# Performance work log

Measured on AMD Instinct MI355X. Metric: run time of the kernel, lower is better.

## Reference

```python
import jax, jax.numpy as jnp
import numpy as np

B, L, H, C = 1, 512, 1024, 2


def setup_inputs() -> dict:
    key = jax.random.key(0)
    k1, k2, k3 = jax.random.split(key, 3)
    lm_output = jax.random.normal(k1, (B, L, H), dtype=jnp.float32)
    # torch Linear weight layout: [out_features, in_features]
    W1 = jax.random.normal(k2, (H, 2 * H), dtype=jnp.float32) * 0.02
    b1 = jnp.zeros((H,), dtype=jnp.float32)
    W2 = jax.random.normal(k3, (C, H), dtype=jnp.float32) * 0.02
    b2 = jnp.zeros((C,), dtype=jnp.float32)
    return {"lm_output": lm_output, "W1": W1, "b1": b1, "W2": W2, "b2": b2}


def reference(lm_output, W1, b1, W2, b2):
    # pair_emb[b,i,j] = concat(lm_output[b,j], lm_output[b,i])
    # Linear(concat(a,b)) decomposes: split W1 into the halves acting on each part.
    Wa = W1[:, :H]  # acts on lm_output_a (the j / column token)
    Wb = W1[:, H:]  # acts on lm_output_b (the i / row token)
    a_proj = jnp.einsum('blh,oh->blo', lm_output, Wa)  # [B,L,H]
    b_proj = jnp.einsum('blh,oh->blo', lm_output, Wb)  # [B,L,H]
    # hidden[b,i,j] = tanh(a_proj[b,j] + b_proj[b,i] + b1)   -> [B,L,L,H]
    hidden = jnp.tanh(a_proj[:, None, :, :] + b_proj[:, :, None, :] + b1)
    # Dropout is identity at inference time.
    logits = jnp.einsum('bijh,ch->bijc', hidden, W2) + b2  # [B,L,L,C]
    logits = (logits + jnp.swapaxes(logits, 1, 2)) / 2.0
    return logits
```

## Files before the change

kernel.cpp:

```cpp
#include <hip/hip_runtime.h>
#include <hip/hip_bf16.h>

#define HH 1024
#define LL 512
#define NT 16
#define NTRI 136

typedef __attribute__((ext_vector_type(8))) short bf16x8;
typedef __attribute__((ext_vector_type(4))) float f32x4;
typedef __attribute__((ext_vector_type(2))) float f32x2;

static constexpr float C_EXP = 2.8853900817779268f;

static __device__ __forceinline__ uint4 pack8(float4 a, float4 b) {
    union { uint4 u; __hip_bfloat162 h[4]; } r;
    r.h[0] = __float22bfloat162_rn(make_float2(a.x, a.y));
    r.h[1] = __float22bfloat162_rn(make_float2(a.z, a.w));
    r.h[2] = __float22bfloat162_rn(make_float2(b.x, b.y));
    r.h[3] = __float22bfloat162_rn(make_float2(b.z, b.w));
    return r.u;
}

__global__ __launch_bounds__(256, 4) void proj_mfma_kernel(
    const float* __restrict__ lm, const float* __restrict__ W1,
    const float* __restrict__ b1, float* __restrict__ Ea, float* __restrict__ Eb)
{
    __shared__ ushort As[64][136];
    __shared__ ushort Bs[64][136];

    const int tid  = threadIdx.x;
    const int lane = tid & 63;
    const int w    = tid >> 6;
    const int b    = blockIdx.x;
    const int xcd  = b & 7;
    const int idx  = b >> 3;
    const int nbase = (xcd * 4 + (idx & 3)) * 64;
    const int mbase = (idx >> 2) * 64;
    const int wm   = w * 16;
    const int sel  = nbase >> 10;
    const int nrow = nbase & 1023;

    const int frow = lane & 15;
    const int q8   = (lane >> 4) * 8;

    f32x4 acc[4] = {};

    for (int kb = 0; kb < HH; kb += 128) {
        __syncthreads();
        {
            int p = tid;
#pragma unroll
            for (int it = 0; it < 4; ++it, p += 256) {
                const int row = p >> 4, c8 = (p & 15) * 8;
                const float* pa = &lm[(mbase + row) * HH + kb + c8];
                *(uint4*)&As[row][c8] = pack8(*(const float4*)pa, *(const float4*)(pa + 4));
                const float* pw = &W1[(nrow + row) * 2048 + sel * 1024 + kb + c8];
                *(uint4*)&Bs[row][c8] = pack8(*(const float4*)pw, *(const float4*)(pw + 4));
            }
        }
        __syncthreads();

#pragma unroll
        for (int s = 0; s < 4; ++s) {
            const bf16x8 a = *(const bf16x8*)&As[wm + frow][s * 32 + q8];
#pragma unroll
            for (int nf = 0; nf < 4; ++nf) {
                const bf16x8 bb = *(const bf16x8*)&Bs[nf * 16 + frow][s * 32 + q8];
                acc[nf] = __builtin_amdgcn_mfma_f32_16x16x32_bf16(a, bb, acc[nf], 0, 0, 0);
            }
        }
    }

    const int col = lane & 15;
    const int rq  = (lane >> 4) * 4;
    const int m0  = mbase + wm + rq;
    const bool isA = sel == 0;
#pragma unroll
    for (int nf = 0; nf < 4; ++nf) {
        const int nn = (nrow + nf * 16 + col);
        if (isA) {
            const float bb = b1[nn];
#pragma unroll
            for (int r = 0; r < 4; ++r)
                Ea[(m0 + r) * HH + nn] = __builtin_amdgcn_exp2f(C_EXP * (acc[nf][r] + bb));
        } else {
#pragma unroll
            for (int r = 0; r < 4; ++r)
                Eb[(m0 + r) * HH + nn] = __builtin_amdgcn_exp2f(C_EXP * acc[nf][r]);
        }
    }
}

__global__ __launch_bounds__(256, 5) void pair_kernel(
    const float* __restrict__ Ea, const float* __restrict__ Eb,
    const float* __restrict__ W2, float* __restrict__ pbuf, int slice)
{
    __shared__ float tl[4][32][64];

    const int tid = threadIdx.x;
    const int tx  = tid & 15;
    const int ty  = tid >> 4;

    int tt = blockIdx.x, bi = 0, rem = NT;
    while (tt >= rem) { tt -= rem; --rem; ++bi; }
    const int bj    = bi + tt;
    const int ibase = bi * 32;
    const int jbase = bj * 32;
    const int k0    = blockIdx.y * slice;

    f32x2 aC0[2] = {}, aC1[2] = {};
    const f32x2 one2 = {1.f, 1.f};

    for (int kb = 0; kb < slice; kb += 64) {
        if (kb) __syncthreads();
        {
            int p = tid;
#pragma unroll
            for (int it = 0; it < 8; ++it, p += 256) {
                const int tile = p >> 9;
                const int row  = (p >> 4) & 31;
                const int c4   = p & 15;
                float4 v;
                if      (tile == 0) v = *(const float4*)&Ea[(jbase + row) * HH + k0 + kb + c4 * 4];
                else if (tile == 1) v = *(const float4*)&Ea[(ibase + row) * HH + k0 + kb + c4 * 4];
                else if (tile == 2) v = *(const float4*)&Eb[(ibase + row) * HH + k0 + kb + c4 * 4];
                else                v = *(const float4*)&Eb[(jbase + row) * HH + k0 + kb + c4 * 4];
                const int c4s = (tile == 0 || tile == 3) ? (c4 ^ (row & 15)) : c4;
                *(float4*)&tl[tile][row][c4s * 4] = v;
            }
        }
        __syncthreads();

#pragma unroll 4
        for (int h4 = 0; h4 < 16; ++h4) {
            const int sx = (h4 ^ tx) * 4;
            const float4 Aj0 = *(const float4*)&tl[0][tx][sx];
            const float4 Aj1 = *(const float4*)&tl[0][tx + 16][sx];
            const float4 Bj0 = *(const float4*)&tl[3][tx][sx];
            const float4 Bj1 = *(const float4*)&tl[3][tx + 16][sx];
            const float4 Ai0 = *(const float4*)&tl[1][ty][h4 * 4];
            const float4 Ai1 = *(const float4*)&tl[1][ty + 16][h4 * 4];
            const float4 Bi0 = *(const float4*)&tl[2][ty][h4 * 4];
            const float4 Bi1 = *(const float4*)&tl[2][ty + 16][h4 * 4];
            const float4 w0q = *(const float4*)&W2[k0 + kb + h4 * 4];
            const float4 w1q = *(const float4*)&W2[HH + k0 + kb + h4 * 4];

#define DO_H(AJ0v, AJ1v, BI0v, BI1v, AI0v, AI1v, BJ0v, BJ1v, W0s, W1s)        \
            {                                                                  \
                const f32x2 Aj = {AJ0v, AJ1v};                                 \
                const f32x2 Bj = {BJ0v, BJ1v};                                 \
                const f32x2 d0 = __builtin_elementwise_fma((f32x2){BI0v, BI0v}, Aj, one2); \
                const f32x2 d1 = __builtin_elementwise_fma((f32x2){BI1v, BI1v}, Aj, one2); \
                const f32x2 e0 = __builtin_elementwise_fma((f32x2){AI0v, AI0v}, Bj, one2); \
                const f32x2 e1 = __builtin_elementwise_fma((f32x2){AI1v, AI1v}, Bj, one2); \
                const float dp0 = d0.x * d0.y, dp1 = d1.x * d1.y;              \
                const float ep0 = e0.x * e0.y, ep1 = e1.x * e1.y;              \
                const float DR = __builtin_amdgcn_rcpf(dp0 * dp1);             \
                const float ER = __builtin_amdgcn_rcpf(ep0 * ep1);             \
                const f32x2 dq = (f32x2){DR, DR} * (f32x2){dp1, dp0};          \
                const f32x2 eq = (f32x2){ER, ER} * (f32x2){ep1, ep0};          \
                const f32x2 u0 = (f32x2){dq.x, dq.x} * d0.yx + (f32x2){eq.x, eq.x} * e0.yx; \
                const f32x2 u1 = (f32x2){dq.y, dq.y} * d1.yx + (f32x2){eq.y, eq.y} * e1.yx; \
                aC0[0] = __builtin_elementwise_fma(u0, (f32x2){(W0s), (W0s)}, aC0[0]); \
                aC1[0] = __builtin_elementwise_fma(u0, (f32x2){(W1s), (W1s)}, aC1[0]); \
                aC0[1] = __builtin_elementwise_fma(u1, (f32x2){(W0s), (W0s)}, aC0[1]); \
                aC1[1] = __builtin_elementwise_fma(u1, (f32x2){(W1s), (W1s)}, aC1[1]); \
            }
            DO_H(Aj0.x, Aj1.x, Bi0.x, Bi1.x, Ai0.x, Ai1.x, Bj0.x, Bj1.x, w0q.x, w1q.x)
            DO_H(Aj0.y, Aj1.y, Bi0.y, Bi1.y, Ai0.y, Ai1.y, Bj0.y, Bj1.y, w0q.y, w1q.y)
            DO_H(Aj0.z, Aj1.z, Bi0.z, Bi1.z, Ai0.z, Ai1.z, Bj0.z, Bj1.z, w0q.z, w1q.z)
            DO_H(Aj0.w, Aj1.w, Bi0.w, Bi1.w, Ai0.w, Ai1.w, Bj0.w, Bj1.w, w0q.w, w1q.w)
#undef DO_H
        }
    }

    float* pb = pbuf + ((size_t)blockIdx.y * NTRI + blockIdx.x) * 2048;
#pragma unroll
    for (int ii = 0; ii < 2; ++ii)
#pragma unroll
        for (int jj = 0; jj < 2; ++jj) {
            const int li = ty + ii * 16, lj = tx + jj * 16;
            const f32x2 v = { jj ? aC0[ii].y : aC0[ii].x,
                              jj ? aC1[ii].y : aC1[ii].x };
            *(f32x2*)&pb[(li * 32 + lj) * 2] = v;
        }
}

__global__ __launch_bounds__(256) void combine_kernel(
    const float* __restrict__ pbuf, const float* __restrict__ W2,
    const float* __restrict__ b2, float* __restrict__ out, int nz)
{
    __shared__ float s_ws[2];

    const int tid = threadIdx.x;
    if (tid < 128) {
        const int c = tid >> 6, l = tid & 63;
        float s = 0.f;
#pragma unroll
        for (int q = 0; q < 4; ++q) {
            const float4 v = *(const float4*)&W2[c * HH + (l + q * 64) * 4];
            s += v.x + v.y + v.z + v.w;
        }
#pragma unroll
        for (int off = 32; off; off >>= 1) s += __shfl_down(s, off, 64);
        if (l == 0) s_ws[c] = s + b2[c];
    }
    __syncthreads();

    const int idx   = blockIdx.x * 256 + tid;
    const int t     = idx >> 11;
    const int local = idx & 2047;
    int tt = t, bi = 0, rem = NT;
    while (tt >= rem) { tt -= rem; --rem; ++bi; }
    const int bj = bi + tt;

    float s0 = 0.f, s1 = 0.f;
    for (int z = 0; z < nz; z += 2) {
        s0 += pbuf[((size_t)z * NTRI + t) * 2048 + local];
        s1 += pbuf[((size_t)(z + 1) * NTRI + t) * 2048 + local];
    }
    const float s = s0 + s1;

    const int li = local >> 6;
    const int lj = (local >> 1) & 31;
    const int c  = local & 1;
    const float v = s_ws[c] - s;

    const int i = bi * 32 + li;
    const int j = bj * 32 + lj;
    out[(i * LL + j) * 2 + c] = v;
    out[(j * LL + i) * 2 + c] = v;
}

extern "C" void kernel_launch(void* const* d_in, const int* in_sizes, int n_in,
                              void* d_out, int out_size, void* d_ws, size_t ws_size,
                              hipStream_t stream)
{
    const float* lm = (const float*)d_in[0];
    const float* W1 = (const float*)d_in[1];
    const float* b1 = (const float*)d_in[2];
    const float* W2 = (const float*)d_in[3];
    const float* b2 = (const float*)d_in[4];
    float* out = (float*)d_out;

    char* ws = (char*)d_ws;
    float* Ea   = (float*)ws;
    float* Eb   = (float*)(ws + (2u << 20));
    float* pbuf = (float*)(ws + (4u << 20) + 64);

    const size_t ubase = (4u << 20) + 64;
    const size_t pb16  = (size_t)16 * NTRI * 2048 * 4;
    const int nz = (ws_size >= ubase + pb16) ? 16 : 8;
    const int slice = HH / nz;

    proj_mfma_kernel<<<256, 256, 0, stream>>>(lm, W1, b1, Ea, Eb);
    pair_kernel<<<dim3(NTRI, nz), 256, 0, stream>>>(Ea, Eb, W2, pbuf, slice);
    combine_kernel<<<(NTRI * 2048) / 256, 256, 0, stream>>>(pbuf, W2, b2, out, nz);
}
```

Before: 129.2 us.

## Enlarge pair tiles to 64x64 with 4x4 register blocking and merged reciprocal

The pair kernel now uses 64x64 triangular tiles (36 tiles) with each thread holding a 4x4 block of pair outputs, where before it used 32x32 tiles (136) with 2x2 per thread. This raises arithmetic reuse per shared-memory load. The tanh-sum formula is regrouped so one reciprocal covers four h values for the symmetric pair. The K split can now go up to 32 slices depending on workspace size, and the combine kernel sums four partials at a time. The cost is higher register pressure (occupancy hint lowered to 3), fewer blocks per slice, and a larger partial buffer for the combine pass to read.

```diff
diff --git a/kernel.cpp b/kernel.cpp
--- a/kernel.cpp
+++ b/kernel.cpp
@@ -3,8 +3,8 @@
 
 #define HH 1024
 #define LL 512
-#define NT 16
-#define NTRI 136
+#define TNT 8
+#define NTILE 36
 
 typedef __attribute__((ext_vector_type(8))) short bf16x8;
 typedef __attribute__((ext_vector_type(4))) float f32x4;
@@ -20,6 +20,9 @@
     r.h[3] = __float22bfloat162_rn(make_float2(b.z, b.w));
     return r.u;
 }
+
+static __device__ __forceinline__ f32x2 lo2(const float4& v) { return (f32x2){v.x, v.y}; }
+static __device__ __forceinline__ f32x2 hi2(const float4& v) { return (f32x2){v.z, v.w}; }
 
 __global__ __launch_bounds__(256, 4) void proj_mfma_kernel(
     const float* __restrict__ lm, const float* __restrict__ W1,
@@ -91,98 +94,105 @@
     }
 }
 
-__global__ __launch_bounds__(256, 5) void pair_kernel(
+__global__ __launch_bounds__(256, 3) void pair_kernel(
     const float* __restrict__ Ea, const float* __restrict__ Eb,
     const float* __restrict__ W2, float* __restrict__ pbuf, int slice)
 {
-    __shared__ float tl[4][32][64];
+    __shared__ float tl[4][64][32];
 
     const int tid = threadIdx.x;
     const int tx  = tid & 15;
     const int ty  = tid >> 4;
 
-    int tt = blockIdx.x, bi = 0, rem = NT;
+    int tt = blockIdx.x, bi = 0, rem = TNT;
     while (tt >= rem) { tt -= rem; --rem; ++bi; }
     const int bj    = bi + tt;
-    const int ibase = bi * 32;
-    const int jbase = bj * 32;
+    const int ibase = bi * 64;
+    const int jbase = bj * 64;
     const int k0    = blockIdx.y * slice;
 
-    f32x2 aC0[2] = {}, aC1[2] = {};
+    f32x2 acc0[4][4] = {};
+    f32x2 acc1[4][4] = {};
     const f32x2 one2 = {1.f, 1.f};
 
-    for (int kb = 0; kb < slice; kb += 64) {
+    for (int kb = 0; kb < slice; kb += 32) {
         if (kb) __syncthreads();
         {
-            int p = tid;
-#pragma unroll
-            for (int it = 0; it < 8; ++it, p += 256) {
-                const int tile = p >> 9;
-                const int row  = (p >> 4) & 31;
-                const int c4   = p & 15;
-                float4 v;
-                if      (tile == 0) v = *(const float4*)&Ea[(jbase + row) * HH + k0 + kb + c4 * 4];
-                else if (tile == 1) v = *(const float4*)&Ea[(ibase + row) * HH + k0 + kb + c4 * 4];
-                else if (tile == 2) v = *(const float4*)&Eb[(ibase + row) * HH + k0 + kb + c4 * 4];
-                else                v = *(const float4*)&Eb[(jbase + row) * HH + k0 + kb + c4 * 4];
-                const int c4s = (tile == 0 || tile == 3) ? (c4 ^ (row & 15)) : c4;
-                *(float4*)&tl[tile][row][c4s * 4] = v;
+            const int c4  = tid & 7;
+            const int r0  = tid >> 3;
+            const int hof = k0 + kb + c4 * 4;
+#pragma unroll
+            for (int it = 0; it < 8; ++it) {
+                const int tile = it >> 1;
+                const int row  = (it & 1) * 32 + r0;
+                const int base = (tile < 2) ? jbase : ibase;
+                const float* src = (tile == 0 || tile == 2) ? Ea : Eb;
+                const int c4s = c4 ^ (row & 7);
+                *(float4*)&tl[tile][row][c4s * 4] =
+                    *(const float4*)&src[(size_t)(base + row) * HH + hof];
             }
         }
         __syncthreads();
 
-#pragma unroll 4
-        for (int h4 = 0; h4 < 16; ++h4) {
-            const int sx = (h4 ^ tx) * 4;
-            const float4 Aj0 = *(const float4*)&tl[0][tx][sx];
-            const float4 Aj1 = *(const float4*)&tl[0][tx + 16][sx];
-            const float4 Bj0 = *(const float4*)&tl[3][tx][sx];
-            const float4 Bj1 = *(const float4*)&tl[3][tx + 16][sx];
-            const float4 Ai0 = *(const float4*)&tl[1][ty][h4 * 4];
-            const float4 Ai1 = *(const float4*)&tl[1][ty + 16][h4 * 4];
-            const float4 Bi0 = *(const float4*)&tl[2][ty][h4 * 4];
-            const float4 Bi1 = *(const float4*)&tl[2][ty + 16][h4 * 4];
+#pragma unroll 2
+        for (int h4 = 0; h4 < 8; ++h4) {
+            const int sxj = (h4 ^ (tx & 7)) * 4;
+            const int sxi = (h4 ^ (ty & 7)) * 4;
+            float4 Aj[4], Bj[4], Ai[4], Bi[4];
+#pragma unroll
+            for (int jj = 0; jj < 4; ++jj) {
+                Aj[jj] = *(const float4*)&tl[0][tx + 16 * jj][sxj];
+                Bj[jj] = *(const float4*)&tl[1][tx + 16 * jj][sxj];
+            }
+#pragma unroll
+            for (int ii = 0; ii < 4; ++ii) {
+                Ai[ii] = *(const float4*)&tl[2][ty + 16 * ii][sxi];
+                Bi[ii] = *(const float4*)&tl[3][ty + 16 * ii][sxi];
+            }
             const float4 w0q = *(const float4*)&W2[k0 + kb + h4 * 4];
             const float4 w1q = *(const float4*)&W2[HH + k0 + kb + h4 * 4];
-
-#define DO_H(AJ0v, AJ1v, BI0v, BI1v, AI0v, AI1v, BJ0v, BJ1v, W0s, W1s)        \
-            {                                                                  \
-                const f32x2 Aj = {AJ0v, AJ1v};                                 \
-                const f32x2 Bj = {BJ0v, BJ1v};                                 \
-                const f32x2 d0 = __builtin_elementwise_fma((f32x2){BI0v, BI0v}, Aj, one2); \
-                const f32x2 d1 = __builtin_elementwise_fma((f32x2){BI1v, BI1v}, Aj, one2); \
-                const f32x2 e0 = __builtin_elementwise_fma((f32x2){AI0v, AI0v}, Bj, one2); \
-                const f32x2 e1 = __builtin_elementwise_fma((f32x2){AI1v, AI1v}, Bj, one2); \
-                const float dp0 = d0.x * d0.y, dp1 = d1.x * d1.y;              \
-                const float ep0 = e0.x * e0.y, ep1 = e1.x * e1.y;              \
-                const float DR = __builtin_amdgcn_rcpf(dp0 * dp1);             \
-                const float ER = __builtin_amdgcn_rcpf(ep0 * ep1);             \
-                const f32x2 dq = (f32x2){DR, DR} * (f32x2){dp1, dp0};          \
-                const f32x2 eq = (f32x2){ER, ER} * (f32x2){ep1, ep0};          \
-                const f32x2 u0 = (f32x2){dq.x, dq.x} * d0.yx + (f32x2){eq.x, eq.x} * e0.yx; \
-                const f32x2 u1 = (f32x2){dq.y, dq.y} * d1.yx + (f32x2){eq.y, eq.y} * e1.yx; \
-                aC0[0] = __builtin_elementwise_fma(u0, (f32x2){(W0s), (W0s)}, aC0[0]); \
-                aC1[0] = __builtin_elementwise_fma(u0, (f32x2){(W1s), (W1s)}, aC1[0]); \
-                aC0[1] = __builtin_elementwise_fma(u1, (f32x2){(W0s), (W0s)}, aC0[1]); \
-                aC1[1] = __builtin_elementwise_fma(u1, (f32x2){(W1s), (W1s)}, aC1[1]); \
-            }
-            DO_H(Aj0.x, Aj1.x, Bi0.x, Bi1.x, Ai0.x, Ai1.x, Bj0.x, Bj1.x, w0q.x, w1q.x)
-            DO_H(Aj0.y, Aj1.y, Bi0.y, Bi1.y, Ai0.y, Ai1.y, Bj0.y, Bj1.y, w0q.y, w1q.y)
-            DO_H(Aj0.z, Aj1.z, Bi0.z, Bi1.z, Ai0.z, Ai1.z, Bj0.z, Bj1.z, w0q.z, w1q.z)
-            DO_H(Aj0.w, Aj1.w, Bi0.w, Bi1.w, Ai0.w, Ai1.w, Bj0.w, Bj1.w, w0q.w, w1q.w)
-#undef DO_H
-        }
-    }
-
-    float* pb = pbuf + ((size_t)blockIdx.y * NTRI + blockIdx.x) * 2048;
-#pragma unroll
-    for (int ii = 0; ii < 2; ++ii)
-#pragma unroll
-        for (int jj = 0; jj < 2; ++jj) {
-            const int li = ty + ii * 16, lj = tx + jj * 16;
-            const f32x2 v = { jj ? aC0[ii].y : aC0[ii].x,
-                              jj ? aC1[ii].y : aC1[ii].x };
-            *(f32x2*)&pb[(li * 32 + lj) * 2] = v;
+            const f32x2 w0lo = lo2(w0q), w0hi = hi2(w0q);
+            const f32x2 w1lo = lo2(w1q), w1hi = hi2(w1q);
+
+#pragma unroll
+            for (int ii = 0; ii < 4; ++ii) {
+                const f32x2 ailo = lo2(Ai[ii]), aihi = hi2(Ai[ii]);
+                const f32x2 bilo = lo2(Bi[ii]), bihi = hi2(Bi[ii]);
+#pragma unroll
+                for (int jj = 0; jj < 4; ++jj) {
+                    const f32x2 d01 = __builtin_elementwise_fma(bilo, lo2(Aj[jj]), one2);
+                    const f32x2 d23 = __builtin_elementwise_fma(bihi, hi2(Aj[jj]), one2);
+                    const f32x2 e01 = __builtin_elementwise_fma(ailo, lo2(Bj[jj]), one2);
+                    const f32x2 e23 = __builtin_elementwise_fma(aihi, hi2(Bj[jj]), one2);
+                    const f32x2 n01 = d01 + e01, n23 = d23 + e23;
+                    const f32x2 m01 = d01 * e01, m23 = d23 * e23;
+                    const float p01 = m01.x * m01.y;
+                    const float p23 = m23.x * m23.y;
+                    const float R   = __builtin_amdgcn_rcpf(p01 * p23);
+                    const float r01 = R * p23;
+                    const float r23 = R * p01;
+                    const f32x2 u01 = (n01 * __builtin_shufflevector(m01, m01, 1, 0))
+                                      * (f32x2){r01, r01};
+                    const f32x2 u23 = (n23 * __builtin_shufflevector(m23, m23, 1, 0))
+                                      * (f32x2){r23, r23};
+                    acc0[ii][jj] = __builtin_elementwise_fma(u01, w0lo, acc0[ii][jj]);
+                    acc0[ii][jj] = __builtin_elementwise_fma(u23, w0hi, acc0[ii][jj]);
+                    acc1[ii][jj] = __builtin_elementwise_fma(u01, w1lo, acc1[ii][jj]);
+                    acc1[ii][jj] = __builtin_elementwise_fma(u23, w1hi, acc1[ii][jj]);
+                }
+            }
+        }
+    }
+
+    float* pb = pbuf + ((size_t)blockIdx.y * NTILE + blockIdx.x) * 8192;
+#pragma unroll
+    for (int ii = 0; ii < 4; ++ii)
+#pragma unroll
+        for (int jj = 0; jj < 4; ++jj) {
+            const int li = ty + 16 * ii, lj = tx + 16 * jj;
+            const f32x2 v = { acc0[ii][jj].x + acc0[ii][jj].y,
+                              acc1[ii][jj].x + acc1[ii][jj].y };
+            *(f32x2*)&pb[(li * 64 + lj) * 2] = v;
         }
 }
 
@@ -208,26 +218,28 @@
     __syncthreads();
 
     const int idx   = blockIdx.x * 256 + tid;
-    const int t     = idx >> 11;
-    const int local = idx & 2047;
-    int tt = t, bi = 0, rem = NT;
+    const int t     = idx >> 13;
+    const int local = idx & 8191;
+    int tt = t, bi = 0, rem = TNT;
     while (tt >= rem) { tt -= rem; --rem; ++bi; }
     const int bj = bi + tt;
 
-    float s0 = 0.f, s1 = 0.f;
-    for (int z = 0; z < nz; z += 2) {
-        s0 += pbuf[((size_t)z * NTRI + t) * 2048 + local];
-        s1 += pbuf[((size_t)(z + 1) * NTRI + t) * 2048 + local];
-    }
-    const float s = s0 + s1;
-
-    const int li = local >> 6;
-    const int lj = (local >> 1) & 31;
+    float s0 = 0.f, s1 = 0.f, s2 = 0.f, s3 = 0.f;
+    for (int z = 0; z < nz; z += 4) {
+        s0 += pbuf[((size_t)z * NTILE + t) * 8192 + local];
+        s1 += pbuf[((size_t)(z + 1) * NTILE + t) * 8192 + local];
+        s2 += pbuf[((size_t)(z + 2) * NTILE + t) * 8192 + local];
+        s3 += pbuf[((size_t)(z + 3) * NTILE + t) * 8192 + local];
+    }
+    const float s = (s0 + s1) + (s2 + s3);
+
+    const int li = local >> 7;
+    const int lj = (local >> 1) & 63;
     const int c  = local & 1;
     const float v = s_ws[c] - s;
 
-    const int i = bi * 32 + li;
-    const int j = bj * 32 + lj;
+    const int i = bi * 64 + li;
+    const int j = bj * 64 + lj;
     out[(i * LL + j) * 2 + c] = v;
     out[(j * LL + i) * 2 + c] = v;
 }
@@ -249,11 +261,13 @@
     float* pbuf = (float*)(ws + (4u << 20) + 64);
 
     const size_t ubase = (4u << 20) + 64;
-    const size_t pb16  = (size_t)16 * NTRI * 2048 * 4;
-    const int nz = (ws_size >= ubase + pb16) ? 16 : 8;
+    const size_t per_z = (size_t)NTILE * 8192 * 4;
+    int nz = 8;
+    if      (ws_size >= ubase + 32 * per_z) nz = 32;
+    else if (ws_size >= ubase + 16 * per_z) nz = 16;
     const int slice = HH / nz;
 
     proj_mfma_kernel<<<256, 256, 0, stream>>>(lm, W1, b1, Ea, Eb);
-    pair_kernel<<<dim3(NTRI, nz), 256, 0, stream>>>(Ea, Eb, W2, pbuf, slice);
-    combine_kernel<<<(NTRI * 2048) / 256, 256, 0, stream>>>(pbuf, W2, b2, out, nz);
-}
+    pair_kernel<<<dim3(NTILE, nz), 256, 0, stream>>>(Ea, Eb, W2, pbuf, slice);
+    combine_kernel<<<(NTILE * 8192) / 256, 256, 0, stream>>>(pbuf, W2, b2, out, nz);
+}
```

Measured after the change: 129.2 us. Within noise of the previous version (-0.0%).

## Regroup tanh-sum algebra per pair and halve projection tile width

Applied to the files above, without the earlier changes.

The pair kernel now computes, for each (i,j) pair, the sum of the two symmetric tanh terms as (d+e)/(d*e), with d and e the two exponential products. One reciprocal is shared across four h values and the paired-vector f32x2 formulation is replaced by scalar accumulators. This is meant to cut the multiplies and reciprocals per hidden element in the dominant loop. Separately, the projection kernel uses 32-wide N tiles and launches 512 blocks instead of 256 to raise parallelism, at the cost of reloading the A tile more often. Pair-kernel occupancy hint and unroll factor are also lowered.

```diff
diff --git a/kernel.cpp b/kernel.cpp
--- a/kernel.cpp
+++ b/kernel.cpp
@@ -26,7 +26,7 @@
     const float* __restrict__ b1, float* __restrict__ Ea, float* __restrict__ Eb)
 {
     __shared__ ushort As[64][136];
-    __shared__ ushort Bs[64][136];
+    __shared__ ushort Bs[32][136];
 
     const int tid  = threadIdx.x;
     const int lane = tid & 63;
@@ -34,8 +34,8 @@
     const int b    = blockIdx.x;
     const int xcd  = b & 7;
     const int idx  = b >> 3;
-    const int nbase = (xcd * 4 + (idx & 3)) * 64;
-    const int mbase = (idx >> 2) * 64;
+    const int nbase = (xcd * 8 + (idx & 7)) * 32;
+    const int mbase = (idx >> 3) * 64;
     const int wm   = w * 16;
     const int sel  = nbase >> 10;
     const int nrow = nbase & 1023;
@@ -43,7 +43,7 @@
     const int frow = lane & 15;
     const int q8   = (lane >> 4) * 8;
 
-    f32x4 acc[4] = {};
+    f32x4 acc[2] = {};
 
     for (int kb = 0; kb < HH; kb += 128) {
         __syncthreads();
@@ -54,6 +54,11 @@
                 const int row = p >> 4, c8 = (p & 15) * 8;
                 const float* pa = &lm[(mbase + row) * HH + kb + c8];
                 *(uint4*)&As[row][c8] = pack8(*(const float4*)pa, *(const float4*)(pa + 4));
+            }
+            int q = tid;
+#pragma unroll
+            for (int it = 0; it < 2; ++it, q += 256) {
+                const int row = q >> 4, c8 = (q & 15) * 8;
                 const float* pw = &W1[(nrow + row) * 2048 + sel * 1024 + kb + c8];
                 *(uint4*)&Bs[row][c8] = pack8(*(const float4*)pw, *(const float4*)(pw + 4));
             }
@@ -64,7 +69,7 @@
         for (int s = 0; s < 4; ++s) {
             const bf16x8 a = *(const bf16x8*)&As[wm + frow][s * 32 + q8];
 #pragma unroll
-            for (int nf = 0; nf < 4; ++nf) {
+            for (int nf = 0; nf < 2; ++nf) {
                 const bf16x8 bb = *(const bf16x8*)&Bs[nf * 16 + frow][s * 32 + q8];
                 acc[nf] = __builtin_amdgcn_mfma_f32_16x16x32_bf16(a, bb, acc[nf], 0, 0, 0);
             }
@@ -76,7 +81,7 @@
     const int m0  = mbase + wm + rq;
     const bool isA = sel == 0;
 #pragma unroll
-    for (int nf = 0; nf < 4; ++nf) {
+    for (int nf = 0; nf < 2; ++nf) {
         const int nn = (nrow + nf * 16 + col);
         if (isA) {
             const float bb = b1[nn];
@@ -91,7 +96,7 @@
     }
 }
 
-__global__ __launch_bounds__(256, 5) void pair_kernel(
+__global__ __launch_bounds__(256, 4) void pair_kernel(
     const float* __restrict__ Ea, const float* __restrict__ Eb,
     const float* __restrict__ W2, float* __restrict__ pbuf, int slice)
 {
@@ -108,8 +113,8 @@
     const int jbase = bj * 32;
     const int k0    = blockIdx.y * slice;
 
-    f32x2 aC0[2] = {}, aC1[2] = {};
-    const f32x2 one2 = {1.f, 1.f};
+    float a00_0 = 0.f, a00_1 = 0.f, a01_0 = 0.f, a01_1 = 0.f;
+    float a10_0 = 0.f, a10_1 = 0.f, a11_0 = 0.f, a11_1 = 0.f;
 
     for (int kb = 0; kb < slice; kb += 64) {
         if (kb) __syncthreads();
@@ -131,7 +136,7 @@
         }
         __syncthreads();
 
-#pragma unroll 4
+#pragma unroll 2
         for (int h4 = 0; h4 < 16; ++h4) {
             const int sx = (h4 ^ tx) * 4;
             const float4 Aj0 = *(const float4*)&tl[0][tx][sx];
@@ -145,45 +150,46 @@
             const float4 w0q = *(const float4*)&W2[k0 + kb + h4 * 4];
             const float4 w1q = *(const float4*)&W2[HH + k0 + kb + h4 * 4];
 
-#define DO_H(AJ0v, AJ1v, BI0v, BI1v, AI0v, AI1v, BJ0v, BJ1v, W0s, W1s)        \
-            {                                                                  \
-                const f32x2 Aj = {AJ0v, AJ1v};                                 \
-                const f32x2 Bj = {BJ0v, BJ1v};                                 \
-                const f32x2 d0 = __builtin_elementwise_fma((f32x2){BI0v, BI0v}, Aj, one2); \
-                const f32x2 d1 = __builtin_elementwise_fma((f32x2){BI1v, BI1v}, Aj, one2); \
-                const f32x2 e0 = __builtin_elementwise_fma((f32x2){AI0v, AI0v}, Bj, one2); \
-                const f32x2 e1 = __builtin_elementwise_fma((f32x2){AI1v, AI1v}, Bj, one2); \
-                const float dp0 = d0.x * d0.y, dp1 = d1.x * d1.y;              \
-                const float ep0 = e0.x * e0.y, ep1 = e1.x * e1.y;              \
-                const float DR = __builtin_amdgcn_rcpf(dp0 * dp1);             \
-                const float ER = __builtin_amdgcn_rcpf(ep0 * ep1);             \
-                const f32x2 dq = (f32x2){DR, DR} * (f32x2){dp1, dp0};          \
-                const f32x2 eq = (f32x2){ER, ER} * (f32x2){ep1, ep0};          \
-                const f32x2 u0 = (f32x2){dq.x, dq.x} * d0.yx + (f32x2){eq.x, eq.x} * e0.yx; \
-                const f32x2 u1 = (f32x2){dq.y, dq.y} * d1.yx + (f32x2){eq.y, eq.y} * e1.yx; \
-                aC0[0] = __builtin_elementwise_fma(u0, (f32x2){(W0s), (W0s)}, aC0[0]); \
-                aC1[0] = __builtin_elementwise_fma(u0, (f32x2){(W1s), (W1s)}, aC1[0]); \
-                aC0[1] = __builtin_elementwise_fma(u1, (f32x2){(W0s), (W0s)}, aC0[1]); \
-                aC1[1] = __builtin_elementwise_fma(u1, (f32x2){(W1s), (W1s)}, aC1[1]); \
-            }
-            DO_H(Aj0.x, Aj1.x, Bi0.x, Bi1.x, Ai0.x, Ai1.x, Bj0.x, Bj1.x, w0q.x, w1q.x)
-            DO_H(Aj0.y, Aj1.y, Bi0.y, Bi1.y, Ai0.y, Ai1.y, Bj0.y, Bj1.y, w0q.y, w1q.y)
-            DO_H(Aj0.z, Aj1.z, Bi0.z, Bi1.z, Ai0.z, Ai1.z, Bj0.z, Bj1.z, w0q.z, w1q.z)
-            DO_H(Aj0.w, Aj1.w, Bi0.w, Bi1.w, Ai0.w, Ai1.w, Bj0.w, Bj1.w, w0q.w, w1q.w)
-#undef DO_H
+#define PAIR(AIv, BIv, AJv, BJv, A0, A1)                                        \
+            {                                                                    \
+                const float d0 = fmaf(BIv.x, AJv.x, 1.f);                        \
+                const float d1 = fmaf(BIv.y, AJv.y, 1.f);                        \
+                const float d2 = fmaf(BIv.z, AJv.z, 1.f);                        \
+                const float d3 = fmaf(BIv.w, AJv.w, 1.f);                        \
+                const float e0 = fmaf(AIv.x, BJv.x, 1.f);                        \
+                const float e1 = fmaf(AIv.y, BJv.y, 1.f);                        \
+                const float e2 = fmaf(AIv.z, BJv.z, 1.f);                        \
+                const float e3 = fmaf(AIv.w, BJv.w, 1.f);                        \
+                const float m0 = d0 * e0, m1 = d1 * e1;                          \
+                const float m2 = d2 * e2, m3 = d3 * e3;                          \
+                const float n0 = d0 + e0, n1 = d1 + e1;                          \
+                const float n2 = d2 + e2, n3 = d3 + e3;                          \
+                const float t01 = m0 * m1, t23 = m2 * m3;                        \
+                const float R  = __builtin_amdgcn_rcpf(t01 * t23);               \
+                const float Ra = R * t23, Rb = R * t01;                          \
+                const float q0 = n0 * m1 * Ra, q1 = n1 * m0 * Ra;                \
+                const float q2 = n2 * m3 * Rb, q3 = n3 * m2 * Rb;                \
+                A0 = fmaf(q0, w0q.x, fmaf(q1, w0q.y,                             \
+                     fmaf(q2, w0q.z, fmaf(q3, w0q.w, A0))));                     \
+                A1 = fmaf(q0, w1q.x, fmaf(q1, w1q.y,                             \
+                     fmaf(q2, w1q.z, fmaf(q3, w1q.w, A1))));                     \
+            }
+            PAIR(Ai0, Bi0, Aj0, Bj0, a00_0, a00_1)
+            PAIR(Ai0, Bi0, Aj1, Bj1, a01_0, a01_1)
+            PAIR(Ai1, Bi1, Aj0, Bj0, a10_0, a10_1)
+            PAIR(Ai1, Bi1, Aj1, Bj1, a11_0, a11_1)
+#undef PAIR
         }
     }
 
     float* pb = pbuf + ((size_t)blockIdx.y * NTRI + blockIdx.x) * 2048;
-#pragma unroll
-    for (int ii = 0; ii < 2; ++ii)
-#pragma unroll
-        for (int jj = 0; jj < 2; ++jj) {
-            const int li = ty + ii * 16, lj = tx + jj * 16;
-            const f32x2 v = { jj ? aC0[ii].y : aC0[ii].x,
-                              jj ? aC1[ii].y : aC1[ii].x };
-            *(f32x2*)&pb[(li * 32 + lj) * 2] = v;
-        }
+    {
+        const int li0 = ty, li1 = ty + 16, lj0 = tx, lj1 = tx + 16;
+        *(f32x2*)&pb[(li0 * 32 + lj0) * 2] = (f32x2){a00_0, a00_1};
+        *(f32x2*)&pb[(li0 * 32 + lj1) * 2] = (f32x2){a01_0, a01_1};
+        *(f32x2*)&pb[(li1 * 32 + lj0) * 2] = (f32x2){a10_0, a10_1};
+        *(f32x2*)&pb[(li1 * 32 + lj1) * 2] = (f32x2){a11_0, a11_1};
+    }
 }
 
 __global__ __launch_bounds__(256) void combine_kernel(
@@ -253,7 +259,7 @@
     const int nz = (ws_size >= ubase + pb16) ? 16 : 8;
     const int slice = HH / nz;
 
-    proj_mfma_kernel<<<256, 256, 0, stream>>>(lm, W1, b1, Ea, Eb);
+    proj_mfma_kernel<<<512, 256, 0, stream>>>(lm, W1, b1, Ea, Eb);
     pair_kernel<<<dim3(NTRI, nz), 256, 0, stream>>>(Ea, Eb, W2, pbuf, slice);
     combine_kernel<<<(NTRI * 2048) / 256, 256, 0, stream>>>(pbuf, W2, b2, out, nz);
 }
```

Result: no change. 129.9 us (+0.6%).

## Shrink projection and pair tiles, add register prefetch in projection GEMM

Applied to the files above, without the earlier changes.

The projection GEMM moves from 64x64 tiles with K-step 128 to 32x32 tiles with K-step 64. It launches four times as many blocks and prefetches the next K-slab into registers while the current slab is computed. The pair kernel halves its shared-memory K-chunk to 32, applies a matching XOR swizzle to all four tiles, and raises its occupancy hint. Together these aim to improve occupancy and latency hiding. In exchange they add more barriers and less reuse per block, and nz is now hard-coded to 16 with no check on workspace size.

```diff
diff --git a/kernel.cpp b/kernel.cpp
--- a/kernel.cpp
+++ b/kernel.cpp
@@ -5,6 +5,7 @@
 #define LL 512
 #define NT 16
 #define NTRI 136
+#define NZ 16
 
 typedef __attribute__((ext_vector_type(8))) short bf16x8;
 typedef __attribute__((ext_vector_type(4))) float f32x4;
@@ -12,7 +13,7 @@
 
 static constexpr float C_EXP = 2.8853900817779268f;
 
-static __device__ __forceinline__ uint4 pack8(float4 a, float4 b) {
+static __device__ __forceinline__ uint4 pack8(f32x4 a, f32x4 b) {
     union { uint4 u; __hip_bfloat162 h[4]; } r;
     r.h[0] = __float22bfloat162_rn(make_float2(a.x, a.y));
     r.h[1] = __float22bfloat162_rn(make_float2(a.z, a.w));
@@ -21,12 +22,12 @@
     return r.u;
 }
 
-__global__ __launch_bounds__(256, 4) void proj_mfma_kernel(
+__global__ __launch_bounds__(256, 8) void proj_mfma_kernel(
     const float* __restrict__ lm, const float* __restrict__ W1,
     const float* __restrict__ b1, float* __restrict__ Ea, float* __restrict__ Eb)
 {
-    __shared__ ushort As[64][136];
-    __shared__ ushort Bs[64][136];
+    __shared__ ushort As[32][72];
+    __shared__ ushort Bs[32][72];
 
     const int tid  = threadIdx.x;
     const int lane = tid & 63;
@@ -34,68 +35,74 @@
     const int b    = blockIdx.x;
     const int xcd  = b & 7;
     const int idx  = b >> 3;
-    const int nbase = (xcd * 4 + (idx & 3)) * 64;
-    const int mbase = (idx >> 2) * 64;
-    const int wm   = w * 16;
+    const int nbase = (xcd * 8 + (idx & 7)) * 32;
+    const int mbase = (idx >> 3) * 32;
+    const int wm   = (w & 1) * 16;
+    const int wn   = (w >> 1) * 16;
     const int sel  = nbase >> 10;
     const int nrow = nbase & 1023;
 
     const int frow = lane & 15;
     const int q8   = (lane >> 4) * 8;
 
-    f32x4 acc[4] = {};
-
-    for (int kb = 0; kb < HH; kb += 128) {
+    const int r0a = tid >> 3;
+    const int c8  = (tid & 7) * 8;
+
+    f32x4 acc = {};
+    f32x4 ld[2][2];
+
+#define PLOAD(kb)                                                              \
+    {                                                                          \
+        const float* pa = &lm[(mbase + r0a) * HH + (kb) + c8];                 \
+        const float* pw = &W1[(nrow + r0a) * 2048 + sel * 1024 + (kb) + c8];   \
+        ld[0][0] = *(const f32x4*)pa; ld[0][1] = *(const f32x4*)(pa + 4);      \
+        ld[1][0] = *(const f32x4*)pw; ld[1][1] = *(const f32x4*)(pw + 4);      \
+    }
+
+#define PSTORE()                                                               \
+    {                                                                          \
+        *(uint4*)&As[r0a][c8] = pack8(ld[0][0], ld[0][1]);                     \
+        *(uint4*)&Bs[r0a][c8] = pack8(ld[1][0], ld[1][1]);                     \
+    }
+
+    PLOAD(0)
+    for (int kb = 0; kb < HH; kb += 64) {
         __syncthreads();
-        {
-            int p = tid;
-#pragma unroll
-            for (int it = 0; it < 4; ++it, p += 256) {
-                const int row = p >> 4, c8 = (p & 15) * 8;
-                const float* pa = &lm[(mbase + row) * HH + kb + c8];
-                *(uint4*)&As[row][c8] = pack8(*(const float4*)pa, *(const float4*)(pa + 4));
-                const float* pw = &W1[(nrow + row) * 2048 + sel * 1024 + kb + c8];
-                *(uint4*)&Bs[row][c8] = pack8(*(const float4*)pw, *(const float4*)(pw + 4));
-            }
-        }
+        PSTORE()
+        if (kb + 64 < HH) PLOAD(kb + 64)
         __syncthreads();
 
 #pragma unroll
-        for (int s = 0; s < 4; ++s) {
-            const bf16x8 a = *(const bf16x8*)&As[wm + frow][s * 32 + q8];
-#pragma unroll
-            for (int nf = 0; nf < 4; ++nf) {
-                const bf16x8 bb = *(const bf16x8*)&Bs[nf * 16 + frow][s * 32 + q8];
-                acc[nf] = __builtin_amdgcn_mfma_f32_16x16x32_bf16(a, bb, acc[nf], 0, 0, 0);
-            }
-        }
-    }
+        for (int s = 0; s < 2; ++s) {
+            const bf16x8 a  = *(const bf16x8*)&As[wm + frow][s * 32 + q8];
+            const bf16x8 bb = *(const bf16x8*)&Bs[wn + frow][s * 32 + q8];
+            acc = __builtin_amdgcn_mfma_f32_16x16x32_bf16(a, bb, acc, 0, 0, 0);
+        }
+    }
+#undef PSTORE
+#undef PLOAD
 
     const int col = lane & 15;
     const int rq  = (lane >> 4) * 4;
     const int m0  = mbase + wm + rq;
-    const bool isA = sel == 0;
-#pragma unroll
-    for (int nf = 0; nf < 4; ++nf) {
-        const int nn = (nrow + nf * 16 + col);
-        if (isA) {
-            const float bb = b1[nn];
-#pragma unroll
-            for (int r = 0; r < 4; ++r)
-                Ea[(m0 + r) * HH + nn] = __builtin_amdgcn_exp2f(C_EXP * (acc[nf][r] + bb));
-        } else {
-#pragma unroll
-            for (int r = 0; r < 4; ++r)
-                Eb[(m0 + r) * HH + nn] = __builtin_amdgcn_exp2f(C_EXP * acc[nf][r]);
-        }
-    }
-}
-
-__global__ __launch_bounds__(256, 5) void pair_kernel(
+    const int nn  = nrow + wn + col;
+    if (sel == 0) {
+        const float bb = b1[nn];
+#pragma unroll
+        for (int r = 0; r < 4; ++r)
+            Ea[(m0 + r) * HH + nn] = __builtin_amdgcn_exp2f(C_EXP * (acc[r] + bb));
+    } else {
+#pragma unroll
+        for (int r = 0; r < 4; ++r)
+            Eb[(m0 + r) * HH + nn] = __builtin_amdgcn_exp2f(C_EXP * acc[r]);
+    }
+}
+
+__global__ __launch_bounds__(256, 6) void pair_kernel(
     const float* __restrict__ Ea, const float* __restrict__ Eb,
     const float* __restrict__ W2, float* __restrict__ pbuf, int slice)
 {
-    __shared__ float tl[4][32][64];
+    __shared__ float tl[4][32][32];
 
     const int tid = threadIdx.x;
     const int tx  = tid & 15;
@@ -111,39 +118,34 @@
     f32x2 aC0[2] = {}, aC1[2] = {};
     const f32x2 one2 = {1.f, 1.f};
 
-    for (int kb = 0; kb < slice; kb += 64) {
+    for (int kb = 0; kb < slice; kb += 32) {
         if (kb) __syncthreads();
         {
-            int p = tid;
-#pragma unroll
-            for (int it = 0; it < 8; ++it, p += 256) {
-                const int tile = p >> 9;
-                const int row  = (p >> 4) & 31;
-                const int c4   = p & 15;
-                float4 v;
-                if      (tile == 0) v = *(const float4*)&Ea[(jbase + row) * HH + k0 + kb + c4 * 4];
-                else if (tile == 1) v = *(const float4*)&Ea[(ibase + row) * HH + k0 + kb + c4 * 4];
-                else if (tile == 2) v = *(const float4*)&Eb[(ibase + row) * HH + k0 + kb + c4 * 4];
-                else                v = *(const float4*)&Eb[(jbase + row) * HH + k0 + kb + c4 * 4];
-                const int c4s = (tile == 0 || tile == 3) ? (c4 ^ (row & 15)) : c4;
-                *(float4*)&tl[tile][row][c4s * 4] = v;
-            }
+            const int row = tid >> 3;
+            const int c4  = tid & 7;
+            const int c4s = c4 ^ (row & 7);
+            const int hof = k0 + kb + c4 * 4;
+            *(f32x4*)&tl[0][row][c4s * 4] = *(const f32x4*)&Ea[(jbase + row) * HH + hof];
+            *(f32x4*)&tl[1][row][c4s * 4] = *(const f32x4*)&Ea[(ibase + row) * HH + hof];
+            *(f32x4*)&tl[2][row][c4s * 4] = *(const f32x4*)&Eb[(ibase + row) * HH + hof];
+            *(f32x4*)&tl[3][row][c4s * 4] = *(const f32x4*)&Eb[(jbase + row) * HH + hof];
         }
         __syncthreads();
 
 #pragma unroll 4
-        for (int h4 = 0; h4 < 16; ++h4) {
-            const int sx = (h4 ^ tx) * 4;
-            const float4 Aj0 = *(const float4*)&tl[0][tx][sx];
-            const float4 Aj1 = *(const float4*)&tl[0][tx + 16][sx];
-            const float4 Bj0 = *(const float4*)&tl[3][tx][sx];
-            const float4 Bj1 = *(const float4*)&tl[3][tx + 16][sx];
-            const float4 Ai0 = *(const float4*)&tl[1][ty][h4 * 4];
-            const float4 Ai1 = *(const float4*)&tl[1][ty + 16][h4 * 4];
-            const float4 Bi0 = *(const float4*)&tl[2][ty][h4 * 4];
-            const float4 Bi1 = *(const float4*)&tl[2][ty + 16][h4 * 4];
-            const float4 w0q = *(const float4*)&W2[k0 + kb + h4 * 4];
-            const float4 w1q = *(const float4*)&W2[HH + k0 + kb + h4 * 4];
+        for (int h4 = 0; h4 < 8; ++h4) {
+            const int sx  = (h4 ^ (tx & 7)) * 4;
+            const int sxi = (h4 ^ (ty & 7)) * 4;
+            const f32x4 Aj0 = *(const f32x4*)&tl[0][tx][sx];
+            const f32x4 Aj1 = *(const f32x4*)&tl[0][tx + 16][sx];
+            const f32x4 Bj0 = *(const f32x4*)&tl[3][tx][sx];
+            const f32x4 Bj1 = *(const f32x4*)&tl[3][tx + 16][sx];
+            const f32x4 Ai0 = *(const f32x4*)&tl[1][ty][sxi];
+            const f32x4 Ai1 = *(const f32x4*)&tl[1][ty + 16][sxi];
+            const f32x4 Bi0 = *(const f32x4*)&tl[2][ty][sxi];
+            const f32x4 Bi1 = *(const f32x4*)&tl[2][ty + 16][sxi];
+            const f32x4 w0q = *(const f32x4*)&W2[k0 + kb + h4 * 4];
+            const f32x4 w1q = *(const f32x4*)&W2[HH + k0 + kb + h4 * 4];
 
 #define DO_H(AJ0v, AJ1v, BI0v, BI1v, AI0v, AI1v, BJ0v, BJ1v, W0s, W1s)        \
             {                                                                  \
@@ -159,8 +161,10 @@
                 const float ER = __builtin_amdgcn_rcpf(ep0 * ep1);             \
                 const f32x2 dq = (f32x2){DR, DR} * (f32x2){dp1, dp0};          \
                 const f32x2 eq = (f32x2){ER, ER} * (f32x2){ep1, ep0};          \
-                const f32x2 u0 = (f32x2){dq.x, dq.x} * d0.yx + (f32x2){eq.x, eq.x} * e0.yx; \
-                const f32x2 u1 = (f32x2){dq.y, dq.y} * d1.yx + (f32x2){eq.y, eq.y} * e1.yx; \
+                const f32x2 u0 = (f32x2){dq.x, dq.x} * __builtin_shufflevector(d0, d0, 1, 0) \
+                               + (f32x2){eq.x, eq.x} * __builtin_shufflevector(e0, e0, 1, 0); \
+                const f32x2 u1 = (f32x2){dq.y, dq.y} * __builtin_shufflevector(d1, d1, 1, 0) \
+                               + (f32x2){eq.y, eq.y} * __builtin_shufflevector(e1, e1, 1, 0); \
                 aC0[0] = __builtin_elementwise_fma(u0, (f32x2){(W0s), (W0s)}, aC0[0]); \
                 aC1[0] = __builtin_elementwise_fma(u0, (f32x2){(W1s), (W1s)}, aC1[0]); \
                 aC0[1] = __builtin_elementwise_fma(u1, (f32x2){(W0s), (W0s)}, aC0[1]); \
@@ -198,7 +202,7 @@
         float s = 0.f;
 #pragma unroll
         for (int q = 0; q < 4; ++q) {
-            const float4 v = *(const float4*)&W2[c * HH + (l + q * 64) * 4];
+            const f32x4 v = *(const f32x4*)&W2[c * HH + (l + q * 64) * 4];
             s += v.x + v.y + v.z + v.w;
         }
 #pragma unroll
@@ -248,12 +252,10 @@
     float* Eb   = (float*)(ws + (2u << 20));
     float* pbuf = (float*)(ws + (4u << 20) + 64);
 
-    const size_t ubase = (4u << 20) + 64;
-    const size_t pb16  = (size_t)16 * NTRI * 2048 * 4;
-    const int nz = (ws_size >= ubase + pb16) ? 16 : 8;
+    const int nz = NZ;
     const int slice = HH / nz;
 
-    proj_mfma_kernel<<<256, 256, 0, stream>>>(lm, W1, b1, Ea, Eb);
+    proj_mfma_kernel<<<1024, 256, 0, stream>>>(lm, W1, b1, Ea, Eb);
     pair_kernel<<<dim3(NTRI, nz), 256, 0, stream>>>(Ea, Eb, W2, pbuf, slice);
     combine_kernel<<<(NTRI * 2048) / 256, 256, 0, stream>>>(pbuf, W2, b2, out, nz);
 }
```

Result: no change. 128.4 us (-0.6%).
